# Kernel tuning notes

Measured on AMD Instinct MI355X. Metric: run time of the kernel, lower is better.

## Reference

```python
import jax, jax.numpy as jnp
import numpy as np

B, LQ, LK = 4, 128, 1024
Q_SIZE, K_SIZE, V_SIZE, UNITS = 512, 512, 512, 256
MASK_VAL = -1e6  # matches torch masked_softmax value=-1000000.0


def setup_inputs() -> dict:
    key = jax.random.key(0)
    ks = jax.random.split(key, 7)
    return {
        "query": jax.random.normal(ks[0], (B, LQ, Q_SIZE), dtype=jnp.float32),
        "key": jax.random.normal(ks[1], (B, LK, K_SIZE), dtype=jnp.float32),
        "value": jax.random.normal(ks[2], (B, LK, V_SIZE), dtype=jnp.float32),
        "valid_len": jax.random.randint(ks[3], (B,), 1, LK + 1).astype(jnp.int64),
        # torch nn.Linear(in, out, bias=False) weight is (out, in)
        "W_q": jax.random.normal(ks[4], (UNITS, Q_SIZE), dtype=jnp.float32) / np.sqrt(Q_SIZE),
        "W_k": jax.random.normal(ks[5], (UNITS, K_SIZE), dtype=jnp.float32) / np.sqrt(K_SIZE),
        "v": jax.random.normal(ks[6], (UNITS,), dtype=jnp.float32) / np.sqrt(UNITS),
    }


def reference(query, key, value, valid_len, W_q, W_k, v):
    # projections: (B,Lq,units), (B,Lk,units)
    q = jnp.einsum("bqd,ud->bqu", query, W_q)
    k = jnp.einsum("bkd,ud->bku", key, W_k)
    # additive features: (B,Lq,Lk,units)
    feats = jnp.tanh(q[:, :, None, :] + k[:, None, :, :])
    # v-projection -> scores (B,Lq,Lk)
    scores = jnp.einsum("bqku,u->bqk", feats, v)
    # mask positions >= valid_len with -1e6 (same as torch sequence_mask)
    mask = jnp.arange(scores.shape[-1]) < valid_len[:, None, None]
    scores = jnp.where(mask, scores, MASK_VAL)
    attn = jax.nn.softmax(scores, axis=-1)  # dropout rate is 0.0
    return jnp.einsum("bqk,bkv->bqv", attn, value)
```

## Files before the change

### kernel.cpp

```cpp
#include <hip/hip_runtime.h>


typedef _Float16 half8 __attribute__((ext_vector_type(8)));
typedef float floatx4 __attribute__((ext_vector_type(4)));

#define EQ_OFF   0
#define EKT_OFF  (512 * 256)

__global__ __launch_bounds__(256) void proj_mfma(
    const float* __restrict__ query, const float* __restrict__ key,
    const float* __restrict__ W_q, const float* __restrict__ W_k,
    const int* __restrict__ vlen, float* __restrict__ Eq,
    float* __restrict__ EkT) {
  __shared__ __align__(16) _Float16 As[64 * 32];
  __shared__ __align__(16) _Float16 Bs[64 * 32];
  const int tid = threadIdx.x;
  const int mb = blockIdx.x;
  const int u0 = blockIdx.y * 64;
  const bool qpart = mb < 8;
  const float *Ag, *Bg;
  int kbatch = 0, j0 = 0, m0 = 0;
  if (qpart) {
    m0 = mb * 64;
    Ag = query + (size_t)m0 * 512;
    Bg = W_q + (size_t)u0 * 512;
  } else {
    const int g0 = (mb - 8) * 64;
    kbatch = g0 >> 10;
    j0 = g0 & 1023;
    if (j0 >= vlen[kbatch]) return;
    Ag = W_k + (size_t)u0 * 512;
    Bg = key + (size_t)g0 * 512;
  }

  const int lrow = tid >> 2, lkq = (tid & 3) * 8;
  const float* Ags = Ag + lrow * 512 + lkq;
  const float* Bgs = Bg + lrow * 512 + lkq;
  _Float16* Ads = As + lrow * 32 + lkq;
  _Float16* Bds = Bs + lrow * 32 + lkq;

  const int lane = tid & 63;
  const int wid = tid >> 6;
  const int wm = (wid & 1) * 32, wn = (wid >> 1) * 32;
  const int frow = lane & 15;
  const int fk = (lane >> 4) * 8;

  floatx4 acc[2][2] = {{{0.f, 0.f, 0.f, 0.f}, {0.f, 0.f, 0.f, 0.f}},
                       {{0.f, 0.f, 0.f, 0.f}, {0.f, 0.f, 0.f, 0.f}}};

  float4 ra0 = *(const float4*)Ags;
  float4 ra1 = *(const float4*)(Ags + 4);
  float4 rb0 = *(const float4*)Bgs;
  float4 rb1 = *(const float4*)(Bgs + 4);

  for (int kb = 0; kb < 16; ++kb) {
    half8 ha, hb;
    ha[0] = (_Float16)ra0.x; ha[1] = (_Float16)ra0.y;
    ha[2] = (_Float16)ra0.z; ha[3] = (_Float16)ra0.w;
    ha[4] = (_Float16)ra1.x; ha[5] = (_Float16)ra1.y;
    ha[6] = (_Float16)ra1.z; ha[7] = (_Float16)ra1.w;
    hb[0] = (_Float16)rb0.x; hb[1] = (_Float16)rb0.y;
    hb[2] = (_Float16)rb0.z; hb[3] = (_Float16)rb0.w;
    hb[4] = (_Float16)rb1.x; hb[5] = (_Float16)rb1.y;
    hb[6] = (_Float16)rb1.z; hb[7] = (_Float16)rb1.w;
    __syncthreads();
    *(half8*)Ads = ha;
    *(half8*)Bds = hb;
    __syncthreads();
    if (kb + 1 < 16) {
      ra0 = *(const float4*)(Ags + (kb + 1) * 32);
      ra1 = *(const float4*)(Ags + (kb + 1) * 32 + 4);
      rb0 = *(const float4*)(Bgs + (kb + 1) * 32);
      rb1 = *(const float4*)(Bgs + (kb + 1) * 32 + 4);
    }
    half8 a0 = *(const half8*)(As + (wm + frow) * 32 + fk);
    half8 a1 = *(const half8*)(As + (wm + 16 + frow) * 32 + fk);
    half8 b0 = *(const half8*)(Bs + (wn + frow) * 32 + fk);
    half8 b1 = *(const half8*)(Bs + (wn + 16 + frow) * 32 + fk);
    acc[0][0] = __builtin_amdgcn_mfma_f32_16x16x32_f16(a0, b0, acc[0][0], 0, 0, 0);
    acc[0][1] = __builtin_amdgcn_mfma_f32_16x16x32_f16(a0, b1, acc[0][1], 0, 0, 0);
    acc[1][0] = __builtin_amdgcn_mfma_f32_16x16x32_f16(a1, b0, acc[1][0], 0, 0, 0);
    acc[1][1] = __builtin_amdgcn_mfma_f32_16x16x32_f16(a1, b1, acc[1][1], 0, 0, 0);
  }

  const int rbase = (lane >> 4) * 4;
  const int col = lane & 15;
#pragma unroll
  for (int mi = 0; mi < 2; ++mi)
#pragma unroll
    for (int ni = 0; ni < 2; ++ni)
#pragma unroll
      for (int r = 0; r < 4; ++r) {
        const int R = wm + mi * 16 + rbase + r;
        const int C = wn + ni * 16 + col;
        const float e = __expf(2.f * acc[mi][ni][r]);
        if (qpart)
          Eq[(m0 + R) * 256 + u0 + C] = e;
        else
          EkT[kbatch * 262144 + (u0 + R) * 1024 + j0 + C] = e;
      }
}

__global__ __launch_bounds__(1024) void scores_attn(
    const float* __restrict__ Eq, const float* __restrict__ EkT,
    const float* __restrict__ vvec, const int* __restrict__ valid_len,
    const float* __restrict__ value, float* __restrict__ out) {
  __shared__ float4 QV[256];
  __shared__ float P0[1024];
  __shared__ float P1[1024];
  __shared__ float2 red[16];
  __shared__ float4 red2[8][2][128];
  const int tid = threadIdx.x;
  const int b = blockIdx.x >> 6;
  const int i0 = (blockIdx.x & 63) * 2;
  const int vl = valid_len[b];

  float vv = 0.f;
  if (tid < 256) {
    vv = vvec[tid];
    QV[tid] = make_float4(Eq[(b * 128 + i0) * 256 + tid],
                          Eq[(b * 128 + i0 + 1) * 256 + tid], -2.f * vv, 0.f);
  }
  float sv = vv;
#pragma unroll
  for (int off = 32; off > 0; off >>= 1) sv += __shfl_xor(sv, off, 64);
  if ((tid & 63) == 0) red[tid >> 6] = make_float2(sv, 0.f);
  __syncthreads();
  float SV = 0.f;
#pragma unroll
  for (int w = 0; w < 16; ++w) SV += red[w].x;

  const int j = tid;
  float p0 = 0.f, p1 = 0.f;
  if (j < vl) {
    float a0 = 0.f, a1 = 0.f;
    const float* kp = EkT + b * 262144 + j;
#pragma unroll 8
    for (int u = 0; u < 256; ++u) {
      float ek = kp[u << 10];
      float4 q = QV[u];
      float r0 = __builtin_amdgcn_rcpf(fmaf(q.x, ek, 1.f));
      float r1 = __builtin_amdgcn_rcpf(fmaf(q.y, ek, 1.f));
      a0 = fmaf(q.z, r0, a0);
      a1 = fmaf(q.z, r1, a1);
    }
    p0 = __expf(SV + a0);
    p1 = __expf(SV + a1);
  }
  P0[j] = p0;
  P1[j] = p1;

  float2 pp = make_float2(p0, p1);
#pragma unroll
  for (int off = 32; off > 0; off >>= 1) {
    pp.x += __shfl_xor(pp.x, off, 64);
    pp.y += __shfl_xor(pp.y, off, 64);
  }
  __syncthreads();
  if ((tid & 63) == 0) red[tid >> 6] = pp;
  __syncthreads();
  float den0 = 0.f, den1 = 0.f;
#pragma unroll
  for (int w = 0; w < 16; ++w) { den0 += red[w].x; den1 += red[w].y; }

  const int cg = tid & 127;
  const int jq = tid >> 7;
  const float* Vb = value + b * 524288 + cg * 4;
  float4 acc0 = make_float4(0.f, 0.f, 0.f, 0.f);
  float4 acc1 = make_float4(0.f, 0.f, 0.f, 0.f);
  const int js = jq * 128;
  const int je = min(js + 128, vl);
  for (int j4 = js; j4 < je; j4 += 4) {
    float4 q0 = *(const float4*)(P0 + j4);
    float4 q1 = *(const float4*)(P1 + j4);
#pragma unroll
    for (int t = 0; t < 4; ++t) {
      float4 v4 = *(const float4*)(Vb + (j4 + t) * 512);
      float w0 = t == 0 ? q0.x : t == 1 ? q0.y : t == 2 ? q0.z : q0.w;
      float w1 = t == 0 ? q1.x : t == 1 ? q1.y : t == 2 ? q1.z : q1.w;
      acc0.x = fmaf(w0, v4.x, acc0.x); acc0.y = fmaf(w0, v4.y, acc0.y);
      acc0.z = fmaf(w0, v4.z, acc0.z); acc0.w = fmaf(w0, v4.w, acc0.w);
      acc1.x = fmaf(w1, v4.x, acc1.x); acc1.y = fmaf(w1, v4.y, acc1.y);
      acc1.z = fmaf(w1, v4.z, acc1.z); acc1.w = fmaf(w1, v4.w, acc1.w);
    }
  }
  red2[jq][0][cg] = acc0;
  red2[jq][1][cg] = acc1;
  __syncthreads();

  if (tid < 256) {
    const int r = tid >> 7, cg2 = tid & 127;
    float4 s = make_float4(0.f, 0.f, 0.f, 0.f);
#pragma unroll
    for (int q = 0; q < 8; ++q) {
      float4 x = red2[q][r][cg2];
      s.x += x.x; s.y += x.y; s.z += x.z; s.w += x.w;
    }
    const float rden = __builtin_amdgcn_rcpf(r ? den1 : den0);
    s.x *= rden; s.y *= rden; s.z *= rden; s.w *= rden;
    *(float4*)(out + (b * 128 + i0 + r) * 512 + cg2 * 4) = s;
  }
}

extern "C" void kernel_launch(void* const* d_in, const int* in_sizes, int n_in,
                              void* d_out, int out_size, void* d_ws, size_t ws_size,
                              hipStream_t stream) {
  const float* query = (const float*)d_in[0];
  const float* key   = (const float*)d_in[1];
  const float* value = (const float*)d_in[2];
  const int*   vlen  = (const int*)d_in[3];
  const float* W_q   = (const float*)d_in[4];
  const float* W_k   = (const float*)d_in[5];
  const float* v     = (const float*)d_in[6];
  float* out = (float*)d_out;

  float* ws  = (float*)d_ws;
  float* Eq  = ws + EQ_OFF;
  float* EkT = ws + EKT_OFF;

  proj_mfma<<<dim3(72, 4), 256, 0, stream>>>(query, key, W_q, W_k, vlen, Eq, EkT);
  scores_attn<<<256, 1024, 0, stream>>>(Eq, EkT, v, vlen, value, out);
}
```

Before: 115.6 us.

## Split attention-weighted value product into separate tiled PV kernel

```diff
diff --git a/kernel.cpp b/kernel.cpp
--- a/kernel.cpp
+++ b/kernel.cpp
@@ -6,6 +6,7 @@
 
 #define EQ_OFF   0
 #define EKT_OFF  (512 * 256)
+#define P_OFF    (512 * 256 + 4 * 256 * 1024)
 
 __global__ __launch_bounds__(256) void proj_mfma(
     const float* __restrict__ query, const float* __restrict__ key,
@@ -101,15 +102,12 @@
       }
 }
 
-__global__ __launch_bounds__(1024) void scores_attn(
+__global__ __launch_bounds__(1024) void scores_exp(
     const float* __restrict__ Eq, const float* __restrict__ EkT,
     const float* __restrict__ vvec, const int* __restrict__ valid_len,
-    const float* __restrict__ value, float* __restrict__ out) {
+    float* __restrict__ P) {
   __shared__ float4 QV[256];
-  __shared__ float P0[1024];
-  __shared__ float P1[1024];
   __shared__ float2 red[16];
-  __shared__ float4 red2[8][2][128];
   const int tid = threadIdx.x;
   const int b = blockIdx.x >> 6;
   const int i0 = (blockIdx.x & 63) * 2;
@@ -147,8 +145,6 @@
     p0 = __expf(SV + a0);
     p1 = __expf(SV + a1);
   }
-  P0[j] = p0;
-  P1[j] = p1;
 
   float2 pp = make_float2(p0, p1);
 #pragma unroll
@@ -163,43 +159,55 @@
 #pragma unroll
   for (int w = 0; w < 16; ++w) { den0 += red[w].x; den1 += red[w].y; }
 
-  const int cg = tid & 127;
-  const int jq = tid >> 7;
-  const float* Vb = value + b * 524288 + cg * 4;
-  float4 acc0 = make_float4(0.f, 0.f, 0.f, 0.f);
-  float4 acc1 = make_float4(0.f, 0.f, 0.f, 0.f);
-  const int js = jq * 128;
-  const int je = min(js + 128, vl);
-  for (int j4 = js; j4 < je; j4 += 4) {
-    float4 q0 = *(const float4*)(P0 + j4);
-    float4 q1 = *(const float4*)(P1 + j4);
-#pragma unroll
-    for (int t = 0; t < 4; ++t) {
-      float4 v4 = *(const float4*)(Vb + (j4 + t) * 512);
-      float w0 = t == 0 ? q0.x : t == 1 ? q0.y : t == 2 ? q0.z : q0.w;
-      float w1 = t == 0 ? q1.x : t == 1 ? q1.y : t == 2 ? q1.z : q1.w;
-      acc0.x = fmaf(w0, v4.x, acc0.x); acc0.y = fmaf(w0, v4.y, acc0.y);
-      acc0.z = fmaf(w0, v4.z, acc0.z); acc0.w = fmaf(w0, v4.w, acc0.w);
-      acc1.x = fmaf(w1, v4.x, acc1.x); acc1.y = fmaf(w1, v4.y, acc1.y);
-      acc1.z = fmaf(w1, v4.z, acc1.z); acc1.w = fmaf(w1, v4.w, acc1.w);
-    }
-  }
-  red2[jq][0][cg] = acc0;
-  red2[jq][1][cg] = acc1;
-  __syncthreads();
-
-  if (tid < 256) {
-    const int r = tid >> 7, cg2 = tid & 127;
-    float4 s = make_float4(0.f, 0.f, 0.f, 0.f);
-#pragma unroll
-    for (int q = 0; q < 8; ++q) {
-      float4 x = red2[q][r][cg2];
-      s.x += x.x; s.y += x.y; s.z += x.z; s.w += x.w;
-    }
-    const float rden = __builtin_amdgcn_rcpf(r ? den1 : den0);
-    s.x *= rden; s.y *= rden; s.z *= rden; s.w *= rden;
-    *(float4*)(out + (b * 128 + i0 + r) * 512 + cg2 * 4) = s;
-  }
+  const float rd0 = __builtin_amdgcn_rcpf(den0);
+  const float rd1 = __builtin_amdgcn_rcpf(den1);
+  float* Pr = P + (size_t)(b * 128 + i0) * 1024 + j;
+  Pr[0] = p0 * rd0;
+  Pr[1024] = p1 * rd1;
+}
+
+__global__ __launch_bounds__(256) void pv_gemm(
+    const float* __restrict__ P, const float* __restrict__ value,
+    const int* __restrict__ valid_len, float* __restrict__ out) {
+  __shared__ float Ps[16 * 1028];
+  const int tid = threadIdx.x;
+  const int ct = blockIdx.x & 7;
+  const int rt = (blockIdx.x >> 3) & 7;
+  const int b  = blockIdx.x >> 6;
+  const int i0 = rt * 16;
+  const int vl = valid_len[b];
+
+  const float* Pg = P + (size_t)(b * 128 + i0) * 1024 + tid * 4;
+#pragma unroll
+  for (int rr = 0; rr < 16; ++rr) {
+    float4 x = *(const float4*)(Pg + rr * 1024);
+    *(float4*)(Ps + rr * 1028 + tid * 4) = x;
+  }
+  __syncthreads();
+
+  const int r = tid >> 4;
+  const int cq = tid & 15;
+  const float* Vp = value + (size_t)b * 524288 + ct * 64 + cq * 4;
+  const float* Pr = Ps + r * 1028;
+  float4 acc = make_float4(0.f, 0.f, 0.f, 0.f);
+  const int vlr = min(1024, (vl + 3) & ~3);
+#pragma unroll 2
+  for (int j = 0; j < vlr; j += 4) {
+    float4 pv = *(const float4*)(Pr + j);
+    float4 v0 = *(const float4*)(Vp + (size_t)(j + 0) * 512);
+    float4 v1 = *(const float4*)(Vp + (size_t)(j + 1) * 512);
+    float4 v2 = *(const float4*)(Vp + (size_t)(j + 2) * 512);
+    float4 v3 = *(const float4*)(Vp + (size_t)(j + 3) * 512);
+    acc.x = fmaf(pv.x, v0.x, acc.x); acc.y = fmaf(pv.x, v0.y, acc.y);
+    acc.z = fmaf(pv.x, v0.z, acc.z); acc.w = fmaf(pv.x, v0.w, acc.w);
+    acc.x = fmaf(pv.y, v1.x, acc.x); acc.y = fmaf(pv.y, v1.y, acc.y);
+    acc.z = fmaf(pv.y, v1.z, acc.z); acc.w = fmaf(pv.y, v1.w, acc.w);
+    acc.x = fmaf(pv.z, v2.x, acc.x); acc.y = fmaf(pv.z, v2.y, acc.y);
+    acc.z = fmaf(pv.z, v2.z, acc.z); acc.w = fmaf(pv.z, v2.w, acc.w);
+    acc.x = fmaf(pv.w, v3.x, acc.x); acc.y = fmaf(pv.w, v3.y, acc.y);
+    acc.z = fmaf(pv.w, v3.z, acc.z); acc.w = fmaf(pv.w, v3.w, acc.w);
+  }
+  *(float4*)(out + (size_t)(b * 128 + i0 + r) * 512 + ct * 64 + cq * 4) = acc;
 }
 
 extern "C" void kernel_launch(void* const* d_in, const int* in_sizes, int n_in,
@@ -217,7 +225,9 @@
   float* ws  = (float*)d_ws;
   float* Eq  = ws + EQ_OFF;
   float* EkT = ws + EKT_OFF;
+  float* P   = ws + P_OFF;
 
   proj_mfma<<<dim3(72, 4), 256, 0, stream>>>(query, key, W_q, W_k, vlen, Eq, EkT);
-  scores_attn<<<256, 1024, 0, stream>>>(Eq, EkT, v, vlen, value, out);
-}
+  scores_exp<<<256, 1024, 0, stream>>>(Eq, EkT, v, vlen, P);
+  pv_gemm<<<256, 256, 0, stream>>>(P, value, vlen, out);
+}
```

Result: slower. 133.2 us (+15.2%).

## Fuse projection and attention kernels into one cooperative kernel with grid sync

Applied to the files above, without the earlier changes.

```diff
diff --git a/kernel.cpp b/kernel.cpp
--- a/kernel.cpp
+++ b/kernel.cpp
@@ -1,5 +1,8 @@
 #include <hip/hip_runtime.h>
-
+#include <hip/hip_cooperative_groups.h>
+
+
+namespace cg = cooperative_groups;
 
 typedef _Float16 half8 __attribute__((ext_vector_type(8)));
 typedef float floatx4 __attribute__((ext_vector_type(4)));
@@ -7,112 +10,138 @@
 #define EQ_OFF   0
 #define EKT_OFF  (512 * 256)
 
-__global__ __launch_bounds__(256) void proj_mfma(
+__global__ __launch_bounds__(1024, 4) void mlp_attn_all(
     const float* __restrict__ query, const float* __restrict__ key,
     const float* __restrict__ W_q, const float* __restrict__ W_k,
-    const int* __restrict__ vlen, float* __restrict__ Eq,
-    float* __restrict__ EkT) {
-  __shared__ __align__(16) _Float16 As[64 * 32];
-  __shared__ __align__(16) _Float16 Bs[64 * 32];
+    const float* __restrict__ vvec, const int* __restrict__ valid_len,
+    const float* __restrict__ value, float* __restrict__ Eq,
+    float* __restrict__ EkT, float* __restrict__ out) {
+  __shared__ __align__(16) char smraw[45184];
+
   const int tid = threadIdx.x;
-  const int mb = blockIdx.x;
-  const int u0 = blockIdx.y * 64;
-  const bool qpart = mb < 8;
-  const float *Ag, *Bg;
-  int kbatch = 0, j0 = 0, m0 = 0;
-  if (qpart) {
-    m0 = mb * 64;
-    Ag = query + (size_t)m0 * 512;
-    Bg = W_q + (size_t)u0 * 512;
-  } else {
-    const int g0 = (mb - 8) * 64;
-    kbatch = g0 >> 10;
-    j0 = g0 & 1023;
-    if (j0 >= vlen[kbatch]) return;
-    Ag = W_k + (size_t)u0 * 512;
-    Bg = key + (size_t)g0 * 512;
-  }
-
-  const int lrow = tid >> 2, lkq = (tid & 3) * 8;
-  const float* Ags = Ag + lrow * 512 + lkq;
-  const float* Bgs = Bg + lrow * 512 + lkq;
-  _Float16* Ads = As + lrow * 32 + lkq;
-  _Float16* Bds = Bs + lrow * 32 + lkq;
-
-  const int lane = tid & 63;
-  const int wid = tid >> 6;
-  const int wm = (wid & 1) * 32, wn = (wid >> 1) * 32;
-  const int frow = lane & 15;
-  const int fk = (lane >> 4) * 8;
-
-  floatx4 acc[2][2] = {{{0.f, 0.f, 0.f, 0.f}, {0.f, 0.f, 0.f, 0.f}},
-                       {{0.f, 0.f, 0.f, 0.f}, {0.f, 0.f, 0.f, 0.f}}};
-
-  float4 ra0 = *(const float4*)Ags;
-  float4 ra1 = *(const float4*)(Ags + 4);
-  float4 rb0 = *(const float4*)Bgs;
-  float4 rb1 = *(const float4*)(Bgs + 4);
-
-  for (int kb = 0; kb < 16; ++kb) {
-    half8 ha, hb;
-    ha[0] = (_Float16)ra0.x; ha[1] = (_Float16)ra0.y;
-    ha[2] = (_Float16)ra0.z; ha[3] = (_Float16)ra0.w;
-    ha[4] = (_Float16)ra1.x; ha[5] = (_Float16)ra1.y;
-    ha[6] = (_Float16)ra1.z; ha[7] = (_Float16)ra1.w;
-    hb[0] = (_Float16)rb0.x; hb[1] = (_Float16)rb0.y;
-    hb[2] = (_Float16)rb0.z; hb[3] = (_Float16)rb0.w;
-    hb[4] = (_Float16)rb1.x; hb[5] = (_Float16)rb1.y;
-    hb[6] = (_Float16)rb1.z; hb[7] = (_Float16)rb1.w;
-    __syncthreads();
-    *(half8*)Ads = ha;
-    *(half8*)Bds = hb;
-    __syncthreads();
-    if (kb + 1 < 16) {
-      ra0 = *(const float4*)(Ags + (kb + 1) * 32);
-      ra1 = *(const float4*)(Ags + (kb + 1) * 32 + 4);
-      rb0 = *(const float4*)(Bgs + (kb + 1) * 32);
-      rb1 = *(const float4*)(Bgs + (kb + 1) * 32 + 4);
-    }
-    half8 a0 = *(const half8*)(As + (wm + frow) * 32 + fk);
-    half8 a1 = *(const half8*)(As + (wm + 16 + frow) * 32 + fk);
-    half8 b0 = *(const half8*)(Bs + (wn + frow) * 32 + fk);
-    half8 b1 = *(const half8*)(Bs + (wn + 16 + frow) * 32 + fk);
-    acc[0][0] = __builtin_amdgcn_mfma_f32_16x16x32_f16(a0, b0, acc[0][0], 0, 0, 0);
-    acc[0][1] = __builtin_amdgcn_mfma_f32_16x16x32_f16(a0, b1, acc[0][1], 0, 0, 0);
-    acc[1][0] = __builtin_amdgcn_mfma_f32_16x16x32_f16(a1, b0, acc[1][0], 0, 0, 0);
-    acc[1][1] = __builtin_amdgcn_mfma_f32_16x16x32_f16(a1, b1, acc[1][1], 0, 0, 0);
-  }
-
-  const int rbase = (lane >> 4) * 4;
-  const int col = lane & 15;
-#pragma unroll
-  for (int mi = 0; mi < 2; ++mi)
-#pragma unroll
-    for (int ni = 0; ni < 2; ++ni)
-#pragma unroll
-      for (int r = 0; r < 4; ++r) {
-        const int R = wm + mi * 16 + rbase + r;
-        const int C = wn + ni * 16 + col;
-        const float e = __expf(2.f * acc[mi][ni][r]);
-        if (qpart)
-          Eq[(m0 + R) * 256 + u0 + C] = e;
-        else
-          EkT[kbatch * 262144 + (u0 + R) * 1024 + j0 + C] = e;
-      }
-}
-
-__global__ __launch_bounds__(1024) void scores_attn(
-    const float* __restrict__ Eq, const float* __restrict__ EkT,
-    const float* __restrict__ vvec, const int* __restrict__ valid_len,
-    const float* __restrict__ value, float* __restrict__ out) {
-  __shared__ float4 QV[256];
-  __shared__ float P0[1024];
-  __shared__ float P1[1024];
-  __shared__ float2 red[16];
-  __shared__ float4 red2[8][2][128];
-  const int tid = threadIdx.x;
-  const int b = blockIdx.x >> 6;
-  const int i0 = (blockIdx.x & 63) * 2;
+  const int bx = blockIdx.x;
+
+  {
+    const int e  = tid >> 8;
+    const int et = tid & 255;
+    const int jid = bx + 256 * e;
+    const bool active = jid < 288;
+    const int mb = jid % 72;
+    const int ub = jid / 72;
+    const int u0 = ub * 64;
+
+    _Float16* As = (_Float16*)smraw + e * 2048;
+    _Float16* Bs = (_Float16*)(smraw + 16384) + e * 2048;
+
+    const float *Ag = query, *Bg = W_q;
+    int kbatch = 0, j0 = 0, m0 = 0;
+    bool qpart = true;
+    if (active) {
+      qpart = mb < 8;
+      if (qpart) {
+        m0 = mb * 64;
+        Ag = query + (size_t)m0 * 512;
+        Bg = W_q + (size_t)u0 * 512;
+      } else {
+        const int g0 = (mb - 8) * 64;
+        kbatch = g0 >> 10;
+        j0 = g0 & 1023;
+        Ag = W_k + (size_t)u0 * 512;
+        Bg = key + (size_t)g0 * 512;
+      }
+    }
+
+    const int lrow = et >> 2, lkq = (et & 3) * 8;
+    const float* Ags = Ag + lrow * 512 + lkq;
+    const float* Bgs = Bg + lrow * 512 + lkq;
+    _Float16* Ads = As + lrow * 32 + lkq;
+    _Float16* Bds = Bs + lrow * 32 + lkq;
+
+    const int wid = (tid >> 6) & 3;
+    const int lane = tid & 63;
+    const int wm = (wid & 1) * 32, wn = (wid >> 1) * 32;
+    const int frow = lane & 15;
+    const int fk = (lane >> 4) * 8;
+
+    floatx4 acc[2][2] = {{{0.f, 0.f, 0.f, 0.f}, {0.f, 0.f, 0.f, 0.f}},
+                         {{0.f, 0.f, 0.f, 0.f}, {0.f, 0.f, 0.f, 0.f}}};
+
+    float4 ra0 = {0, 0, 0, 0}, ra1 = {0, 0, 0, 0};
+    float4 rb0 = {0, 0, 0, 0}, rb1 = {0, 0, 0, 0};
+    if (active) {
+      ra0 = *(const float4*)Ags;
+      ra1 = *(const float4*)(Ags + 4);
+      rb0 = *(const float4*)Bgs;
+      rb1 = *(const float4*)(Bgs + 4);
+    }
+
+    for (int kb = 0; kb < 16; ++kb) {
+      half8 ha = {0, 0, 0, 0, 0, 0, 0, 0}, hb = {0, 0, 0, 0, 0, 0, 0, 0};
+      if (active) {
+        ha[0] = (_Float16)ra0.x; ha[1] = (_Float16)ra0.y;
+        ha[2] = (_Float16)ra0.z; ha[3] = (_Float16)ra0.w;
+        ha[4] = (_Float16)ra1.x; ha[5] = (_Float16)ra1.y;
+        ha[6] = (_Float16)ra1.z; ha[7] = (_Float16)ra1.w;
+        hb[0] = (_Float16)rb0.x; hb[1] = (_Float16)rb0.y;
+        hb[2] = (_Float16)rb0.z; hb[3] = (_Float16)rb0.w;
+        hb[4] = (_Float16)rb1.x; hb[5] = (_Float16)rb1.y;
+        hb[6] = (_Float16)rb1.z; hb[7] = (_Float16)rb1.w;
+      }
+      __syncthreads();
+      if (active) {
+        *(half8*)Ads = ha;
+        *(half8*)Bds = hb;
+      }
+      __syncthreads();
+      if (active) {
+        if (kb + 1 < 16) {
+          ra0 = *(const float4*)(Ags + (kb + 1) * 32);
+          ra1 = *(const float4*)(Ags + (kb + 1) * 32 + 4);
+          rb0 = *(const float4*)(Bgs + (kb + 1) * 32);
+          rb1 = *(const float4*)(Bgs + (kb + 1) * 32 + 4);
+        }
+        half8 a0 = *(const half8*)(As + (wm + frow) * 32 + fk);
+        half8 a1 = *(const half8*)(As + (wm + 16 + frow) * 32 + fk);
+        half8 b0 = *(const half8*)(Bs + (wn + frow) * 32 + fk);
+        half8 b1 = *(const half8*)(Bs + (wn + 16 + frow) * 32 + fk);
+        acc[0][0] = __builtin_amdgcn_mfma_f32_16x16x32_f16(a0, b0, acc[0][0], 0, 0, 0);
+        acc[0][1] = __builtin_amdgcn_mfma_f32_16x16x32_f16(a0, b1, acc[0][1], 0, 0, 0);
+        acc[1][0] = __builtin_amdgcn_mfma_f32_16x16x32_f16(a1, b0, acc[1][0], 0, 0, 0);
+        acc[1][1] = __builtin_amdgcn_mfma_f32_16x16x32_f16(a1, b1, acc[1][1], 0, 0, 0);
+      }
+    }
+
+    if (active) {
+      const int rbase = (lane >> 4) * 4;
+      const int col = lane & 15;
+#pragma unroll
+      for (int mi = 0; mi < 2; ++mi)
+#pragma unroll
+        for (int ni = 0; ni < 2; ++ni)
+#pragma unroll
+          for (int r = 0; r < 4; ++r) {
+            const int R = wm + mi * 16 + rbase + r;
+            const int C = wn + ni * 16 + col;
+            const float eo = __expf(2.f * acc[mi][ni][r]);
+            if (qpart)
+              Eq[(m0 + R) * 256 + u0 + C] = eo;
+            else
+              EkT[kbatch * 262144 + (u0 + R) * 1024 + j0 + C] = eo;
+          }
+    }
+  }
+
+  __threadfence();
+  cg::this_grid().sync();
+
+  float4* QV = (float4*)smraw;
+  float*  P0 = (float*)(smraw + 4096);
+  float*  P1 = (float*)(smraw + 8192);
+  float2* red = (float2*)(smraw + 12288);
+  float4* red2 = (float4*)(smraw + 12416);
+
+  const int b = bx >> 6;
+  const int i0 = (bx & 63) * 2;
   const int vl = valid_len[b];
 
   float vv = 0.f;
@@ -163,9 +192,9 @@
 #pragma unroll
   for (int w = 0; w < 16; ++w) { den0 += red[w].x; den1 += red[w].y; }
 
-  const int cg = tid & 127;
+  const int cg2i = tid & 127;
   const int jq = tid >> 7;
-  const float* Vb = value + b * 524288 + cg * 4;
+  const float* Vb = value + b * 524288 + cg2i * 4;
   float4 acc0 = make_float4(0.f, 0.f, 0.f, 0.f);
   float4 acc1 = make_float4(0.f, 0.f, 0.f, 0.f);
   const int js = jq * 128;
@@ -184,21 +213,21 @@
       acc1.z = fmaf(w1, v4.z, acc1.z); acc1.w = fmaf(w1, v4.w, acc1.w);
     }
   }
-  red2[jq][0][cg] = acc0;
-  red2[jq][1][cg] = acc1;
+  red2[(jq * 2 + 0) * 128 + cg2i] = acc0;
+  red2[(jq * 2 + 1) * 128 + cg2i] = acc1;
   __syncthreads();
 
   if (tid < 256) {
-    const int r = tid >> 7, cg2 = tid & 127;
+    const int r = tid >> 7, cg3 = tid & 127;
     float4 s = make_float4(0.f, 0.f, 0.f, 0.f);
 #pragma unroll
     for (int q = 0; q < 8; ++q) {
-      float4 x = red2[q][r][cg2];
+      float4 x = red2[(q * 2 + r) * 128 + cg3];
       s.x += x.x; s.y += x.y; s.z += x.z; s.w += x.w;
     }
     const float rden = __builtin_amdgcn_rcpf(r ? den1 : den0);
     s.x *= rden; s.y *= rden; s.z *= rden; s.w *= rden;
-    *(float4*)(out + (b * 128 + i0 + r) * 512 + cg2 * 4) = s;
+    *(float4*)(out + (b * 128 + i0 + r) * 512 + cg3 * 4) = s;
   }
 }
 
@@ -218,6 +247,9 @@
   float* Eq  = ws + EQ_OFF;
   float* EkT = ws + EKT_OFF;
 
-  proj_mfma<<<dim3(72, 4), 256, 0, stream>>>(query, key, W_q, W_k, vlen, Eq, EkT);
-  scores_attn<<<256, 1024, 0, stream>>>(Eq, EkT, v, vlen, value, out);
+  void* args[10] = {(void*)&query, (void*)&key,  (void*)&W_q, (void*)&W_k,
+                    (void*)&v,     (void*)&vlen, (void*)&value,
+                    (void*)&Eq,    (void*)&EkT,  (void*)&out};
+  hipLaunchCooperativeKernel((const void*)mlp_attn_all, dim3(256), dim3(1024),
+                             args, 0, stream);
 }
```

After: 231.6 us. 2x slower.
